# Performance work log

Measured on AMD Instinct MI355X. Metric: run time of the kernel, lower is better.

## Reference

```python
import jax, jax.numpy as jnp
import numpy as np

BATCH, DIM, HEADS = 512, 2048, 16
CPH = DIM // HEADS  # per-head channels = 128
EPS = 1e-5


def setup_inputs() -> dict:
    key = jax.random.key(0)
    ks = jax.random.split(key, 6)
    x = jax.random.normal(ks[0], (BATCH, DIM, 1, 1), dtype=jnp.float32)
    W_qv = jax.random.normal(ks[1], (2 * DIM, DIM), dtype=jnp.float32) * (1.0 / np.sqrt(DIM))
    temperature = jnp.ones((HEADS, 1, 1), dtype=jnp.float32)
    k_param = jax.random.normal(ks[2], (BATCH, DIM, 1, 1), dtype=jnp.float32)
    bias_param = jax.random.normal(ks[3], (BATCH, HEADS, CPH * CPH, 1), dtype=jnp.float32)
    bn_gamma = jnp.ones((HEADS,), dtype=jnp.float32)
    bn_beta = jnp.zeros((HEADS,), dtype=jnp.float32)
    W_out = jax.random.normal(ks[4], (DIM, DIM, 1, 1), dtype=jnp.float32) * (1.0 / np.sqrt(DIM))
    b_out = jax.random.normal(ks[5], (DIM,), dtype=jnp.float32) * 0.01
    return {"x": x, "W_qv": W_qv, "temperature": temperature, "k_param": k_param,
            "bias_param": bias_param, "bn_gamma": bn_gamma, "bn_beta": bn_beta,
            "W_out": W_out, "b_out": b_out}


def reference(x, W_qv, temperature, k_param, bias_param, bn_gamma, bn_beta, W_out, b_out):
    b, c, h, w = x.shape  # h = w = 1 (required by x.squeeze() + Linear)
    heads = temperature.shape[0]
    cph = c // heads

    xs = x.reshape(b, c)
    qv = xs @ W_qv.T                     # [b, 2c]
    q, v = qv[:, :c], qv[:, c:]
    q = q.reshape(b, heads, cph, 1)      # b head c (h w)
    v = v.reshape(b, heads, cph, 1)
    k = k_param.reshape(b, heads, cph, 1)

    # BatchNorm2d over channel = head (training-mode batch stats, biased var)
    mean = jnp.mean(v, axis=(0, 2, 3), keepdims=True)
    var = jnp.var(v, axis=(0, 2, 3), keepdims=True)
    v = (v - mean) * jax.lax.rsqrt(var + EPS)
    v = v * bn_gamma.reshape(1, heads, 1, 1) + bn_beta.reshape(1, heads, 1, 1)

    # attn = q @ k^T over the singleton spatial dim -> [b, head, cph, cph]
    attn = jnp.einsum('bhcx,bhdx->bhcd', q, k)
    attn = attn + bias_param.reshape(b, heads, cph, cph)
    attn = attn * temperature  # [heads,1,1] broadcasts over batch
    attn = jax.nn.softmax(attn, axis=-1)

    out = jnp.einsum('bhcd,bhdx->bhcx', attn, v)  # [b, head, cph, 1]
    out = out.reshape(b, c)

    # 1x1 conv == matmul
    out = out @ W_out.reshape(c, c).T + b_out
    return out.reshape(b, c, 1, 1)
```

## Files before the change

### kernel.cpp

```cpp
#include <hip/hip_runtime.h>
#include <hip/hip_bf16.h>
#include <cstdint>

#define NBATCH 512
#define NDIM   2048
#define NHEADS 16
#define NCPH   128

typedef __bf16 bf16x8 __attribute__((ext_vector_type(8)));
typedef float  f32x4  __attribute__((ext_vector_type(4)));

__device__ __forceinline__ unsigned short f2bf(float f) {
    uint32_t u = __builtin_bit_cast(uint32_t, f);
    u += 0x7FFFu + ((u >> 16) & 1u);
    return (unsigned short)(u >> 16);
}

__device__ __forceinline__ void gl_lds16(const void* g, void* l) {
    __builtin_amdgcn_global_load_lds(
        (const __attribute__((address_space(1))) void*)g,
        (__attribute__((address_space(3))) void*)l,
        16, 0, 0);
}

template<int BM, int BN, int BK, bool A_BF16, bool BNP>
__global__ __launch_bounds__(256) void gemm_f(
    const unsigned short* __restrict__ Abf, const float* __restrict__ Af,
    const float* __restrict__ Bf, float* __restrict__ C,
    const float* __restrict__ bias, float* __restrict__ bnpart,
    int M, int N, int K)
{
    constexpr int WM = BM / 2, WN = BN / 2;
    constexpr int MI = WM / 16, NI = WN / 16;
    constexpr int CPR = BK / 8;
    constexpr int RA = (BM * BK) / 8 / 256;
    constexpr int GA = (BM * BK) / 2048;
    constexpr int RB = (BN * BK) / 8 / 256;

    __shared__ unsigned short As[2][BM * BK];
    __shared__ unsigned short Bs[2][BN * BK];

    const int tid  = threadIdx.x;
    const int lane = tid & 63;
    const int wid  = tid >> 6;
    const int wr   = wid >> 1;
    const int wc   = wid & 1;
    const int m0   = blockIdx.y * BM;
    const int n0   = blockIdx.x * BN;
    const int fr   = lane & 15;
    const int kq   = lane >> 4;

    f32x4 acc[MI][NI] = {};
    float4 rga[RA > 0 ? RA : 1][2], rgb[RB][2];

    auto load_A = [&](int bs, int k0) {
        if constexpr (A_BF16) {
#pragma unroll
            for (int r = 0; r < GA; r++) {
                const int e   = r * 2048 + tid * 8;
                const int row = e / BK;
                const int swz = ((((e & (BK - 1)) >> 3) ^ (row & 7)) << 3);
                gl_lds16(Abf + (size_t)(m0 + row) * K + k0 + swz, &As[bs][e]);
            }
        } else {
#pragma unroll
            for (int r = 0; r < RA; r++) {
                const int idx = r * 256 + tid;
                const int row = idx / CPR, cc = idx % CPR;
                const float4* g = (const float4*)(Af + (size_t)(m0 + row) * K
                                                  + k0 + cc * 8);
                rga[r][0] = g[0];
                rga[r][1] = g[1];
            }
        }
    };
    auto load_B = [&](int k0) {
#pragma unroll
        for (int r = 0; r < RB; r++) {
            const int idx = r * 256 + tid;
            const int row = idx / CPR, cc = idx % CPR;
            const float4* g = (const float4*)(Bf + (size_t)(n0 + row) * K
                                              + k0 + cc * 8);
            rgb[r][0] = g[0];
            rgb[r][1] = g[1];
        }
    };
    auto write_A = [&](int bs) {
        if constexpr (!A_BF16) {
#pragma unroll
            for (int r = 0; r < RA; r++) {
                const int idx = r * 256 + tid;
                const int row = idx / CPR, cc = idx % CPR;
                bf16x8 v;
                v[0] = (__bf16)rga[r][0].x; v[1] = (__bf16)rga[r][0].y;
                v[2] = (__bf16)rga[r][0].z; v[3] = (__bf16)rga[r][0].w;
                v[4] = (__bf16)rga[r][1].x; v[5] = (__bf16)rga[r][1].y;
                v[6] = (__bf16)rga[r][1].z; v[7] = (__bf16)rga[r][1].w;
                *(bf16x8*)&As[bs][row * BK + ((cc ^ (row & 7)) << 3)] = v;
            }
        }
    };
    auto write_B = [&](int bs) {
#pragma unroll
        for (int r = 0; r < RB; r++) {
            const int idx = r * 256 + tid;
            const int row = idx / CPR, cc = idx % CPR;
            bf16x8 v;
            v[0] = (__bf16)rgb[r][0].x; v[1] = (__bf16)rgb[r][0].y;
            v[2] = (__bf16)rgb[r][0].z; v[3] = (__bf16)rgb[r][0].w;
            v[4] = (__bf16)rgb[r][1].x; v[5] = (__bf16)rgb[r][1].y;
            v[6] = (__bf16)rgb[r][1].z; v[7] = (__bf16)rgb[r][1].w;
            *(bf16x8*)&Bs[bs][row * BK + ((cc ^ (row & 7)) << 3)] = v;
        }
    };
    auto compute = [&](int bs) {
#pragma unroll
        for (int kh = 0; kh < BK / 32; kh++) {
            const int kchunk = kh * 4 + kq;
            bf16x8 af[MI], bfv[NI];
#pragma unroll
            for (int i = 0; i < MI; i++) {
                const int row = wr * WM + i * 16 + fr;
                af[i] = *(const bf16x8*)&As[bs][row * BK
                        + ((kchunk ^ (row & 7)) << 3)];
            }
#pragma unroll
            for (int j = 0; j < NI; j++) {
                const int row = wc * WN + j * 16 + fr;
                bfv[j] = *(const bf16x8*)&Bs[bs][row * BK
                         + ((kchunk ^ (row & 7)) << 3)];
            }
#pragma unroll
            for (int i = 0; i < MI; i++)
#pragma unroll
                for (int j = 0; j < NI; j++)
                    acc[i][j] = __builtin_amdgcn_mfma_f32_16x16x32_bf16(
                        af[i], bfv[j], acc[i][j], 0, 0, 0);
        }
    };

    load_A(0, 0);
    load_B(0);
    write_A(0);
    write_B(0);
    __syncthreads();

    const int NT = K / BK;
    int cur = 0;
    for (int t = 0; t < NT - 1; t++) {
        load_A(cur ^ 1, (t + 1) * BK);
        load_B((t + 1) * BK);
        compute(cur);
        write_A(cur ^ 1);
        write_B(cur ^ 1);
        __syncthreads();
        cur ^= 1;
    }
    compute(cur);

    const int row0 = m0 + wr * WM + (kq << 2);
    const int col0 = n0 + wc * WN + fr;
#pragma unroll
    for (int j = 0; j < NI; j++) {
        const int cc = col0 + j * 16;
        const float badd = bias ? bias[cc] : 0.0f;
#pragma unroll
        for (int i = 0; i < MI; i++)
#pragma unroll
            for (int r = 0; r < 4; r++)
                C[(size_t)(row0 + i * 16 + r) * N + cc] = acc[i][j][r] + badd;
    }

    if (BNP && n0 >= NDIM) {
        float s = 0.f, ss = 0.f;
#pragma unroll
        for (int i = 0; i < MI; i++)
#pragma unroll
            for (int j = 0; j < NI; j++)
#pragma unroll
                for (int r = 0; r < 4; r++) {
                    const float v = acc[i][j][r];
                    s += v;
                    ss = fmaf(v, v, ss);
                }
#pragma unroll
        for (int off = 32; off; off >>= 1) {
            s  += __shfl_down(s, off);
            ss += __shfl_down(ss, off);
        }
        __shared__ float rs[4], rss[4];
        if (lane == 0) { rs[wid] = s; rss[wid] = ss; }
        __syncthreads();
        if (tid == 0)
            ((float2*)bnpart)[((n0 - NDIM) >> 6) * 8 + (m0 >> 6)] =
                make_float2(rs[0] + rs[1] + rs[2] + rs[3],
                            rss[0] + rss[1] + rss[2] + rss[3]);
    }
}

__global__ __launch_bounds__(256) void attn_k(
    const float* __restrict__ qv, const float* __restrict__ kparam,
    const float* __restrict__ bias, const float* __restrict__ temperature,
    const float* __restrict__ bnpart, const float* __restrict__ gamma,
    const float* __restrict__ beta, unsigned short* __restrict__ aout)
{
    const int bh = blockIdx.x;
    const int b  = bh >> 4;
    const int h  = bh & 15;
    const int tid = threadIdx.x;

    __shared__ float ks[NCPH], vsr[NCPH], s2sh[2];
    if (tid < 32)
        ((float4*)ks)[tid] =
            ((const float4*)(kparam + (size_t)b * NDIM + h * NCPH))[tid];
    else if (tid < 64)
        ((float4*)vsr)[tid - 32] =
            ((const float4*)(qv + (size_t)b * (2 * NDIM) + NDIM + h * NCPH))[tid - 32];

    if (tid < 16) {
        float2 p = ((const float2*)bnpart)[(h * 2 + (tid >> 3)) * 8 + (tid & 7)];
        float s = p.x, ss = p.y;
#pragma unroll
        for (int off = 8; off; off >>= 1) {
            s  += __shfl_xor(s, off);
            ss += __shfl_xor(ss, off);
        }
        if (tid == 0) {
            const float inv = 1.0f / (NBATCH * NCPH);
            float mean = s * inv;
            float var  = ss * inv - mean * mean;
            float sc   = gamma[h] * rsqrtf(var + 1e-5f);
            s2sh[0] = sc;
            s2sh[1] = beta[h] - mean * sc;
        }
    }

    const int c = tid >> 1, half = tid & 1;
    const float qc   = qv[(size_t)b * (2 * NDIM) + h * NCPH + c];
    const float temp = temperature[h];

    const float4* bp = (const float4*)(bias + ((size_t)bh << 14)
                                       + (size_t)c * NCPH + half * 64);
    float4 l4[16];
#pragma unroll
    for (int j = 0; j < 16; j++) l4[j] = bp[j];

    __syncthreads();
    const float sc = s2sh[0], sh = s2sh[1];
    const float4* kk4 = (const float4*)(ks  + half * 64);
    const float4* vv4 = (const float4*)(vsr + half * 64);

    float s0 = 0.f, s1 = 0.f, o0 = 0.f, o1 = 0.f;
#pragma unroll
    for (int j = 0; j < 16; j++) {
        const float4 bb = l4[j];
        const float4 kx = kk4[j];
        const float4 vx = vv4[j];
        float px = __expf(fmaf(qc, kx.x, bb.x) * temp);
        float py = __expf(fmaf(qc, kx.y, bb.y) * temp);
        float pz = __expf(fmaf(qc, kx.z, bb.z) * temp);
        float pw = __expf(fmaf(qc, kx.w, bb.w) * temp);
        s0 += px; s1 += py; s0 += pz; s1 += pw;
        o0 = fmaf(px, vx.x, o0);
        o1 = fmaf(py, vx.y, o1);
        o0 = fmaf(pz, vx.z, o0);
        o1 = fmaf(pw, vx.w, o1);
    }
    float s = s0 + s1, o = o0 + o1;
    s += __shfl_xor(s, 1);
    o += __shfl_xor(o, 1);

    if (half == 0)
        aout[(size_t)b * NDIM + h * NCPH + c] = f2bf(fmaf(sc, o / s, sh));
}

extern "C" void kernel_launch(void* const* d_in, const int* in_sizes, int n_in,
                              void* d_out, int out_size, void* d_ws, size_t ws_size,
                              hipStream_t stream)
{
    const float* x      = (const float*)d_in[0];
    const float* Wqv    = (const float*)d_in[1];
    const float* temp   = (const float*)d_in[2];
    const float* kparam = (const float*)d_in[3];
    const float* bias   = (const float*)d_in[4];
    const float* gamma  = (const float*)d_in[5];
    const float* beta   = (const float*)d_in[6];
    const float* Wout   = (const float*)d_in[7];
    const float* bout   = (const float*)d_in[8];
    float* out = (float*)d_out;

    char* ws = (char*)d_ws;
    float*          qv     = (float*)(ws);
    unsigned short* ao_bf  = (unsigned short*)(ws + 8388608);
    float*          bnpart = (float*)(ws + 10485760);

    gemm_f<64, 64, 64, false, true><<<dim3(64, 8), 256, 0, stream>>>(
        nullptr, x, Wqv, qv, nullptr, bnpart, NBATCH, 2 * NDIM, NDIM);

    attn_k<<<NBATCH * NHEADS, 256, 0, stream>>>(
        qv, kparam, bias, temp, bnpart, gamma, beta, ao_bf);

    gemm_f<64, 32, 64, true, false><<<dim3(64, 8), 256, 0, stream>>>(
        ao_bf, nullptr, Wout, out, bout, nullptr, NBATCH, NDIM, NDIM);
}
```

Before: 165.0 us.

## Deepen GEMM prefetch to two register stages and split attention rows across blocks

The GEMM kernel now keeps two sets of prefetch registers, so global loads for tile t+2 and t+3 are in flight while tiles t and t+1 are computed. It uses a custom barrier (lgkmcnt wait, s_barrier and sched_barrier) in place of __syncthreads. The bf16 A path moves from direct global-to-LDS loads to register loads followed by swizzled LDS writes. The attention kernel launches twice as many blocks, each covering 64 rows with four threads per row, for more parallelism and fewer registers per thread. The cost is higher register pressure in the GEMM and redundant k/v/BN-stat loading in attention.

```diff
diff --git a/kernel.cpp b/kernel.cpp
--- a/kernel.cpp
+++ b/kernel.cpp
@@ -16,15 +16,8 @@
     return (unsigned short)(u >> 16);
 }
 
-__device__ __forceinline__ void gl_lds16(const void* g, void* l) {
-    __builtin_amdgcn_global_load_lds(
-        (const __attribute__((address_space(1))) void*)g,
-        (__attribute__((address_space(3))) void*)l,
-        16, 0, 0);
-}
-
 template<int BM, int BN, int BK, bool A_BF16, bool BNP>
-__global__ __launch_bounds__(256) void gemm_f(
+__global__ __launch_bounds__(256) void gemm_deep(
     const unsigned short* __restrict__ Abf, const float* __restrict__ Af,
     const float* __restrict__ Bf, float* __restrict__ C,
     const float* __restrict__ bias, float* __restrict__ bnpart,
@@ -33,9 +26,8 @@
     constexpr int WM = BM / 2, WN = BN / 2;
     constexpr int MI = WM / 16, NI = WN / 16;
     constexpr int CPR = BK / 8;
-    constexpr int RA = (BM * BK) / 8 / 256;
-    constexpr int GA = (BM * BK) / 2048;
-    constexpr int RB = (BN * BK) / 8 / 256;
+    constexpr int RNA = (BM * BK) / 2048;
+    constexpr int RNB = (BN * BK) / 2048;
 
     __shared__ unsigned short As[2][BM * BK];
     __shared__ unsigned short Bs[2][BN * BK];
@@ -51,65 +43,74 @@
     const int kq   = lane >> 4;
 
     f32x4 acc[MI][NI] = {};
-    float4 rga[RA > 0 ? RA : 1][2], rgb[RB][2];
-
-    auto load_A = [&](int bs, int k0) {
+
+    float4 fA0[A_BF16 ? 1 : RNA][2], fA1[A_BF16 ? 1 : RNA][2];
+    bf16x8 hA0[A_BF16 ? RNA : 1],    hA1[A_BF16 ? RNA : 1];
+    float4 fB0[RNB][2], fB1[RNB][2];
+
+    auto loadA = [&](auto& fa, auto& ha, int k0) {
         if constexpr (A_BF16) {
 #pragma unroll
-            for (int r = 0; r < GA; r++) {
-                const int e   = r * 2048 + tid * 8;
-                const int row = e / BK;
-                const int swz = ((((e & (BK - 1)) >> 3) ^ (row & 7)) << 3);
-                gl_lds16(Abf + (size_t)(m0 + row) * K + k0 + swz, &As[bs][e]);
+            for (int r = 0; r < RNA; r++) {
+                const int e = r * 2048 + tid * 8;
+                const int row = e / BK, cb = e % BK;
+                ha[r] = *(const bf16x8*)(Abf + (size_t)(m0 + row) * K + k0 + cb);
             }
         } else {
 #pragma unroll
-            for (int r = 0; r < RA; r++) {
+            for (int r = 0; r < RNA; r++) {
                 const int idx = r * 256 + tid;
                 const int row = idx / CPR, cc = idx % CPR;
                 const float4* g = (const float4*)(Af + (size_t)(m0 + row) * K
                                                   + k0 + cc * 8);
-                rga[r][0] = g[0];
-                rga[r][1] = g[1];
-            }
-        }
-    };
-    auto load_B = [&](int k0) {
-#pragma unroll
-        for (int r = 0; r < RB; r++) {
+                fa[r][0] = g[0];
+                fa[r][1] = g[1];
+            }
+        }
+    };
+    auto loadB = [&](auto& fb, int k0) {
+#pragma unroll
+        for (int r = 0; r < RNB; r++) {
             const int idx = r * 256 + tid;
             const int row = idx / CPR, cc = idx % CPR;
             const float4* g = (const float4*)(Bf + (size_t)(n0 + row) * K
                                               + k0 + cc * 8);
-            rgb[r][0] = g[0];
-            rgb[r][1] = g[1];
-        }
-    };
-    auto write_A = [&](int bs) {
-        if constexpr (!A_BF16) {
-#pragma unroll
-            for (int r = 0; r < RA; r++) {
+            fb[r][0] = g[0];
+            fb[r][1] = g[1];
+        }
+    };
+    auto writeA = [&](int bs, auto& fa, auto& ha) {
+        if constexpr (A_BF16) {
+#pragma unroll
+            for (int r = 0; r < RNA; r++) {
+                const int e = r * 2048 + tid * 8;
+                const int row = e / BK, cc = (e % BK) >> 3;
+                *(bf16x8*)&As[bs][row * BK + ((cc ^ (row & 7)) << 3)] = ha[r];
+            }
+        } else {
+#pragma unroll
+            for (int r = 0; r < RNA; r++) {
                 const int idx = r * 256 + tid;
                 const int row = idx / CPR, cc = idx % CPR;
                 bf16x8 v;
-                v[0] = (__bf16)rga[r][0].x; v[1] = (__bf16)rga[r][0].y;
-                v[2] = (__bf16)rga[r][0].z; v[3] = (__bf16)rga[r][0].w;
-                v[4] = (__bf16)rga[r][1].x; v[5] = (__bf16)rga[r][1].y;
-                v[6] = (__bf16)rga[r][1].z; v[7] = (__bf16)rga[r][1].w;
+                v[0] = (__bf16)fa[r][0].x; v[1] = (__bf16)fa[r][0].y;
+                v[2] = (__bf16)fa[r][0].z; v[3] = (__bf16)fa[r][0].w;
+                v[4] = (__bf16)fa[r][1].x; v[5] = (__bf16)fa[r][1].y;
+                v[6] = (__bf16)fa[r][1].z; v[7] = (__bf16)fa[r][1].w;
                 *(bf16x8*)&As[bs][row * BK + ((cc ^ (row & 7)) << 3)] = v;
             }
         }
     };
-    auto write_B = [&](int bs) {
-#pragma unroll
-        for (int r = 0; r < RB; r++) {
+    auto writeB = [&](int bs, auto& fb) {
+#pragma unroll
+        for (int r = 0; r < RNB; r++) {
             const int idx = r * 256 + tid;
             const int row = idx / CPR, cc = idx % CPR;
             bf16x8 v;
-            v[0] = (__bf16)rgb[r][0].x; v[1] = (__bf16)rgb[r][0].y;
-            v[2] = (__bf16)rgb[r][0].z; v[3] = (__bf16)rgb[r][0].w;
-            v[4] = (__bf16)rgb[r][1].x; v[5] = (__bf16)rgb[r][1].y;
-            v[6] = (__bf16)rgb[r][1].z; v[7] = (__bf16)rgb[r][1].w;
+            v[0] = (__bf16)fb[r][0].x; v[1] = (__bf16)fb[r][0].y;
+            v[2] = (__bf16)fb[r][0].z; v[3] = (__bf16)fb[r][0].w;
+            v[4] = (__bf16)fb[r][1].x; v[5] = (__bf16)fb[r][1].y;
+            v[6] = (__bf16)fb[r][1].z; v[7] = (__bf16)fb[r][1].w;
             *(bf16x8*)&Bs[bs][row * BK + ((cc ^ (row & 7)) << 3)] = v;
         }
     };
@@ -138,25 +139,35 @@
                         af[i], bfv[j], acc[i][j], 0, 0, 0);
         }
     };
-
-    load_A(0, 0);
-    load_B(0);
-    write_A(0);
-    write_B(0);
-    __syncthreads();
+    auto barrier = [&]() {
+        asm volatile("s_waitcnt lgkmcnt(0)" ::: "memory");
+        __builtin_amdgcn_s_barrier();
+        __builtin_amdgcn_sched_barrier(0);
+    };
+
+    loadA(fA0, hA0, 0);
+    loadB(fB0, 0);
+    loadA(fA1, hA1, BK);
+    loadB(fB1, BK);
+    writeA(0, fA0, hA0);
+    writeB(0, fB0);
+    barrier();
 
     const int NT = K / BK;
-    int cur = 0;
-    for (int t = 0; t < NT - 1; t++) {
-        load_A(cur ^ 1, (t + 1) * BK);
-        load_B((t + 1) * BK);
-        compute(cur);
-        write_A(cur ^ 1);
-        write_B(cur ^ 1);
-        __syncthreads();
-        cur ^= 1;
-    }
-    compute(cur);
+    for (int t = 0; t < NT; t += 2) {
+        if (t + 2 < NT) { loadA(fA0, hA0, (t + 2) * BK); loadB(fB0, (t + 2) * BK); }
+        compute(0);
+        writeA(1, fA1, hA1);
+        writeB(1, fB1);
+        barrier();
+        if (t + 3 < NT) { loadA(fA1, hA1, (t + 3) * BK); loadB(fB1, (t + 3) * BK); }
+        compute(1);
+        if (t + 2 < NT) {
+            writeA(0, fA0, hA0);
+            writeB(0, fB0);
+            barrier();
+        }
+    }
 
     const int row0 = m0 + wr * WM + (kq << 2);
     const int col0 = n0 + wc * WN + fr;
@@ -204,9 +215,9 @@
     const float* __restrict__ bnpart, const float* __restrict__ gamma,
     const float* __restrict__ beta, unsigned short* __restrict__ aout)
 {
-    const int bh = blockIdx.x;
-    const int b  = bh >> 4;
-    const int h  = bh & 15;
+    const int bh2 = blockIdx.x;
+    const int bh  = bh2 >> 1, rh = bh2 & 1;
+    const int b   = bh >> 4,  h  = bh & 15;
     const int tid = threadIdx.x;
 
     __shared__ float ks[NCPH], vsr[NCPH], s2sh[2];
@@ -229,30 +240,31 @@
             const float inv = 1.0f / (NBATCH * NCPH);
             float mean = s * inv;
             float var  = ss * inv - mean * mean;
-            float sc   = gamma[h] * rsqrtf(var + 1e-5f);
-            s2sh[0] = sc;
-            s2sh[1] = beta[h] - mean * sc;
-        }
-    }
-
-    const int c = tid >> 1, half = tid & 1;
+            float scl  = gamma[h] * rsqrtf(var + 1e-5f);
+            s2sh[0] = scl;
+            s2sh[1] = beta[h] - mean * scl;
+        }
+    }
+
+    const int c  = rh * 64 + (tid >> 2);
+    const int q4 = tid & 3;
     const float qc   = qv[(size_t)b * (2 * NDIM) + h * NCPH + c];
     const float temp = temperature[h];
 
     const float4* bp = (const float4*)(bias + ((size_t)bh << 14)
-                                       + (size_t)c * NCPH + half * 64);
-    float4 l4[16];
-#pragma unroll
-    for (int j = 0; j < 16; j++) l4[j] = bp[j];
+                                       + (size_t)c * NCPH + q4 * 32);
+    float4 l4[8];
+#pragma unroll
+    for (int j = 0; j < 8; j++) l4[j] = bp[j];
 
     __syncthreads();
-    const float sc = s2sh[0], sh = s2sh[1];
-    const float4* kk4 = (const float4*)(ks  + half * 64);
-    const float4* vv4 = (const float4*)(vsr + half * 64);
+    const float scl = s2sh[0], shf = s2sh[1];
+    const float4* kk4 = (const float4*)(ks  + q4 * 32);
+    const float4* vv4 = (const float4*)(vsr + q4 * 32);
 
     float s0 = 0.f, s1 = 0.f, o0 = 0.f, o1 = 0.f;
 #pragma unroll
-    for (int j = 0; j < 16; j++) {
+    for (int j = 0; j < 8; j++) {
         const float4 bb = l4[j];
         const float4 kx = kk4[j];
         const float4 vx = vv4[j];
@@ -269,9 +281,11 @@
     float s = s0 + s1, o = o0 + o1;
     s += __shfl_xor(s, 1);
     o += __shfl_xor(o, 1);
-
-    if (half == 0)
-        aout[(size_t)b * NDIM + h * NCPH + c] = f2bf(fmaf(sc, o / s, sh));
+    s += __shfl_xor(s, 2);
+    o += __shfl_xor(o, 2);
+
+    if (q4 == 0)
+        aout[(size_t)b * NDIM + h * NCPH + c] = f2bf(fmaf(scl, o / s, shf));
 }
 
 extern "C" void kernel_launch(void* const* d_in, const int* in_sizes, int n_in,
@@ -294,12 +308,12 @@
     unsigned short* ao_bf  = (unsigned short*)(ws + 8388608);
     float*          bnpart = (float*)(ws + 10485760);
 
-    gemm_f<64, 64, 64, false, true><<<dim3(64, 8), 256, 0, stream>>>(
+    gemm_deep<64, 64, 64, false, true><<<dim3(64, 8), 256, 0, stream>>>(
         nullptr, x, Wqv, qv, nullptr, bnpart, NBATCH, 2 * NDIM, NDIM);
 
-    attn_k<<<NBATCH * NHEADS, 256, 0, stream>>>(
+    attn_k<<<2 * NBATCH * NHEADS, 256, 0, stream>>>(
         qv, kparam, bias, temp, bnpart, gamma, beta, ao_bf);
 
-    gemm_f<64, 32, 64, true, false><<<dim3(64, 8), 256, 0, stream>>>(
+    gemm_deep<64, 32, 64, true, false><<<dim3(64, 8), 256, 0, stream>>>(
         ao_bf, nullptr, Wout, out, bout, nullptr, NBATCH, NDIM, NDIM);
 }
```

New measurement: 165.8 us. Within noise of the previous version (+0.5%).

## Pre-convert x to bf16 and use tall BM=128 GEMM tiles with narrow N

Applied to the files above, without the earlier changes.

A new kernel converts x to bf16 up front, so the QV GEMM can load A straight into LDS with global_load_lds instead of converting it in registers. Both GEMMs move to a tall tile layout (BM=128, four warps stacked along M, BN of 32 or 16). Each block then reads a smaller slice of the fp32 weights, so the weight traffic is spread over more blocks. The BatchNorm partial-sum indexing is updated to match the new tile grid. This costs an extra kernel launch and an extra x round trip through memory, and the narrow N tiles reuse A less.

```diff
diff --git a/kernel.cpp b/kernel.cpp
--- a/kernel.cpp
+++ b/kernel.cpp
@@ -8,6 +8,7 @@
 #define NCPH   128
 
 typedef __bf16 bf16x8 __attribute__((ext_vector_type(8)));
+typedef __bf16 bf16x4 __attribute__((ext_vector_type(4)));
 typedef float  f32x4  __attribute__((ext_vector_type(4)));
 
 __device__ __forceinline__ unsigned short f2bf(float f) {
@@ -23,19 +24,28 @@
         16, 0, 0);
 }
 
-template<int BM, int BN, int BK, bool A_BF16, bool BNP>
-__global__ __launch_bounds__(256) void gemm_f(
-    const unsigned short* __restrict__ Abf, const float* __restrict__ Af,
-    const float* __restrict__ Bf, float* __restrict__ C,
-    const float* __restrict__ bias, float* __restrict__ bnpart,
-    int M, int N, int K)
-{
-    constexpr int WM = BM / 2, WN = BN / 2;
-    constexpr int MI = WM / 16, NI = WN / 16;
-    constexpr int CPR = BK / 8;
-    constexpr int RA = (BM * BK) / 8 / 256;
+__global__ __launch_bounds__(256) void cvt_x(
+    const float* __restrict__ x, unsigned short* __restrict__ ox)
+{
+    const int t = blockIdx.x * 256 + threadIdx.x;
+    float4 v = ((const float4*)x)[t];
+    ushort4 o;
+    o.x = f2bf(v.x); o.y = f2bf(v.y); o.z = f2bf(v.z); o.w = f2bf(v.w);
+    ((ushort4*)ox)[t] = o;
+}
+
+template<int BN, int BK, bool BNP>
+__global__ __launch_bounds__(256) void gemm_tall(
+    const unsigned short* __restrict__ Abf, const float* __restrict__ Bf,
+    float* __restrict__ C, const float* __restrict__ bias,
+    float* __restrict__ bnpart, int M, int N, int K)
+{
+    constexpr int BM = 128;
+    constexpr int MI = 2;
+    constexpr int NI = BN / 16;
     constexpr int GA = (BM * BK) / 2048;
-    constexpr int RB = (BN * BK) / 8 / 256;
+    constexpr int BPT4 = (BN * BK) / 1024;
+    constexpr int CPRB = BK / 8;
 
     __shared__ unsigned short As[2][BM * BK];
     __shared__ unsigned short Bs[2][BN * BK];
@@ -43,74 +53,53 @@
     const int tid  = threadIdx.x;
     const int lane = tid & 63;
     const int wid  = tid >> 6;
-    const int wr   = wid >> 1;
-    const int wc   = wid & 1;
     const int m0   = blockIdx.y * BM;
     const int n0   = blockIdx.x * BN;
     const int fr   = lane & 15;
     const int kq   = lane >> 4;
 
     f32x4 acc[MI][NI] = {};
-    float4 rga[RA > 0 ? RA : 1][2], rgb[RB][2];
-
-    auto load_A = [&](int bs, int k0) {
-        if constexpr (A_BF16) {
-#pragma unroll
-            for (int r = 0; r < GA; r++) {
-                const int e   = r * 2048 + tid * 8;
-                const int row = e / BK;
-                const int swz = ((((e & (BK - 1)) >> 3) ^ (row & 7)) << 3);
-                gl_lds16(Abf + (size_t)(m0 + row) * K + k0 + swz, &As[bs][e]);
-            }
+    float4 rb[BPT4];
+
+    const int brow = (BPT4 == 2) ? tid / CPRB : tid >> 4;
+    const int bch  = (BPT4 == 2) ? tid % CPRB : ((tid & 15) >> 1);
+    const int bhalf = (BPT4 == 2) ? 0 : (tid & 1);
+
+    auto loadA = [&](int bs, int k0) {
+#pragma unroll
+        for (int r = 0; r < GA; r++) {
+            const int e    = r * 2048 + tid * 8;
+            const int row  = e / BK;
+            const int chk  = (e % BK) >> 3;
+            gl_lds16(Abf + (size_t)(m0 + row) * K + k0
+                         + ((chk ^ (row & 7)) << 3), &As[bs][e]);
+        }
+    };
+    auto loadB = [&](int k0) {
+        if constexpr (BPT4 == 2) {
+            const float4* g = (const float4*)(Bf + (size_t)(n0 + brow) * K
+                                              + k0 + bch * 8);
+            rb[0] = g[0];
+            rb[1] = g[1];
         } else {
-#pragma unroll
-            for (int r = 0; r < RA; r++) {
-                const int idx = r * 256 + tid;
-                const int row = idx / CPR, cc = idx % CPR;
-                const float4* g = (const float4*)(Af + (size_t)(m0 + row) * K
-                                                  + k0 + cc * 8);
-                rga[r][0] = g[0];
-                rga[r][1] = g[1];
-            }
-        }
-    };
-    auto load_B = [&](int k0) {
-#pragma unroll
-        for (int r = 0; r < RB; r++) {
-            const int idx = r * 256 + tid;
-            const int row = idx / CPR, cc = idx % CPR;
-            const float4* g = (const float4*)(Bf + (size_t)(n0 + row) * K
-                                              + k0 + cc * 8);
-            rgb[r][0] = g[0];
-            rgb[r][1] = g[1];
-        }
-    };
-    auto write_A = [&](int bs) {
-        if constexpr (!A_BF16) {
-#pragma unroll
-            for (int r = 0; r < RA; r++) {
-                const int idx = r * 256 + tid;
-                const int row = idx / CPR, cc = idx % CPR;
-                bf16x8 v;
-                v[0] = (__bf16)rga[r][0].x; v[1] = (__bf16)rga[r][0].y;
-                v[2] = (__bf16)rga[r][0].z; v[3] = (__bf16)rga[r][0].w;
-                v[4] = (__bf16)rga[r][1].x; v[5] = (__bf16)rga[r][1].y;
-                v[6] = (__bf16)rga[r][1].z; v[7] = (__bf16)rga[r][1].w;
-                *(bf16x8*)&As[bs][row * BK + ((cc ^ (row & 7)) << 3)] = v;
-            }
-        }
-    };
-    auto write_B = [&](int bs) {
-#pragma unroll
-        for (int r = 0; r < RB; r++) {
-            const int idx = r * 256 + tid;
-            const int row = idx / CPR, cc = idx % CPR;
+            rb[0] = *(const float4*)(Bf + (size_t)(n0 + brow) * K + k0
+                                     + bch * 8 + bhalf * 4);
+        }
+    };
+    auto writeB = [&](int bs) {
+        const int base = brow * BK + ((bch ^ (brow & 7)) << 3);
+        if constexpr (BPT4 == 2) {
             bf16x8 v;
-            v[0] = (__bf16)rgb[r][0].x; v[1] = (__bf16)rgb[r][0].y;
-            v[2] = (__bf16)rgb[r][0].z; v[3] = (__bf16)rgb[r][0].w;
-            v[4] = (__bf16)rgb[r][1].x; v[5] = (__bf16)rgb[r][1].y;
-            v[6] = (__bf16)rgb[r][1].z; v[7] = (__bf16)rgb[r][1].w;
-            *(bf16x8*)&Bs[bs][row * BK + ((cc ^ (row & 7)) << 3)] = v;
+            v[0] = (__bf16)rb[0].x; v[1] = (__bf16)rb[0].y;
+            v[2] = (__bf16)rb[0].z; v[3] = (__bf16)rb[0].w;
+            v[4] = (__bf16)rb[1].x; v[5] = (__bf16)rb[1].y;
+            v[6] = (__bf16)rb[1].z; v[7] = (__bf16)rb[1].w;
+            *(bf16x8*)&Bs[bs][base] = v;
+        } else {
+            bf16x4 v;
+            v[0] = (__bf16)rb[0].x; v[1] = (__bf16)rb[0].y;
+            v[2] = (__bf16)rb[0].z; v[3] = (__bf16)rb[0].w;
+            *(bf16x4*)&Bs[bs][base + bhalf * 4] = v;
         }
     };
     auto compute = [&](int bs) {
@@ -120,13 +109,13 @@
             bf16x8 af[MI], bfv[NI];
 #pragma unroll
             for (int i = 0; i < MI; i++) {
-                const int row = wr * WM + i * 16 + fr;
+                const int row = wid * 32 + i * 16 + fr;
                 af[i] = *(const bf16x8*)&As[bs][row * BK
                         + ((kchunk ^ (row & 7)) << 3)];
             }
 #pragma unroll
             for (int j = 0; j < NI; j++) {
-                const int row = wc * WN + j * 16 + fr;
+                const int row = j * 16 + fr;
                 bfv[j] = *(const bf16x8*)&Bs[bs][row * BK
                          + ((kchunk ^ (row & 7)) << 3)];
             }
@@ -139,27 +128,25 @@
         }
     };
 
-    load_A(0, 0);
-    load_B(0);
-    write_A(0);
-    write_B(0);
+    loadA(0, 0);
+    loadB(0);
+    writeB(0);
     __syncthreads();
 
     const int NT = K / BK;
     int cur = 0;
     for (int t = 0; t < NT - 1; t++) {
-        load_A(cur ^ 1, (t + 1) * BK);
-        load_B((t + 1) * BK);
+        loadB((t + 1) * BK);
+        loadA(cur ^ 1, (t + 1) * BK);
         compute(cur);
-        write_A(cur ^ 1);
-        write_B(cur ^ 1);
+        writeB(cur ^ 1);
         __syncthreads();
         cur ^= 1;
     }
     compute(cur);
 
-    const int row0 = m0 + wr * WM + (kq << 2);
-    const int col0 = n0 + wc * WN + fr;
+    const int row0 = m0 + wid * 32 + (kq << 2);
+    const int col0 = n0 + fr;
 #pragma unroll
     for (int j = 0; j < NI; j++) {
         const int cc = col0 + j * 16;
@@ -192,7 +179,7 @@
         if (lane == 0) { rs[wid] = s; rss[wid] = ss; }
         __syncthreads();
         if (tid == 0)
-            ((float2*)bnpart)[((n0 - NDIM) >> 6) * 8 + (m0 >> 6)] =
+            ((float2*)bnpart)[((n0 - NDIM) >> 5) * 4 + (m0 >> 7)] =
                 make_float2(rs[0] + rs[1] + rs[2] + rs[3],
                             rss[0] + rss[1] + rss[2] + rss[3]);
     }
@@ -218,7 +205,7 @@
             ((const float4*)(qv + (size_t)b * (2 * NDIM) + NDIM + h * NCPH))[tid - 32];
 
     if (tid < 16) {
-        float2 p = ((const float2*)bnpart)[(h * 2 + (tid >> 3)) * 8 + (tid & 7)];
+        float2 p = ((const float2*)bnpart)[h * 16 + tid];
         float s = p.x, ss = p.y;
 #pragma unroll
         for (int off = 8; off; off >>= 1) {
@@ -293,13 +280,16 @@
     float*          qv     = (float*)(ws);
     unsigned short* ao_bf  = (unsigned short*)(ws + 8388608);
     float*          bnpart = (float*)(ws + 10485760);
-
-    gemm_f<64, 64, 64, false, true><<<dim3(64, 8), 256, 0, stream>>>(
-        nullptr, x, Wqv, qv, nullptr, bnpart, NBATCH, 2 * NDIM, NDIM);
+    unsigned short* x_bf   = (unsigned short*)(ws + 10487808);
+
+    cvt_x<<<1024, 256, 0, stream>>>(x, x_bf);
+
+    gemm_tall<32, 64, true><<<dim3(128, 4), 256, 0, stream>>>(
+        x_bf, Wqv, qv, nullptr, bnpart, NBATCH, 2 * NDIM, NDIM);
 
     attn_k<<<NBATCH * NHEADS, 256, 0, stream>>>(
         qv, kparam, bias, temp, bnpart, gamma, beta, ao_bf);
 
-    gemm_f<64, 32, 64, true, false><<<dim3(64, 8), 256, 0, stream>>>(
-        ao_bf, nullptr, Wout, out, bout, nullptr, NBATCH, NDIM, NDIM);
-}
+    gemm_tall<16, 64, false><<<dim3(128, 4), 256, 0, stream>>>(
+        ao_bf, Wout, out, bout, nullptr, NBATCH, NDIM, NDIM);
+}
```

After: 184.8 us. 1.12x slower.
